# Kernel tuning notes

Measured on AMD Instinct MI355X. Metric: run time of the kernel, lower is better.

The kernel has to match this reference:

```python
import jax, jax.numpy as jnp
import numpy as np

D_MODEL = 512
N_HEADS = 8
HEAD_DIM = D_MODEL // N_HEADS
SCALE = float(np.sqrt(HEAD_DIM))


def setup_inputs() -> dict:
    key = jax.random.key(0)
    k1, k2, k3, k4, k5, k6 = jax.random.split(key, 6)
    B, T, S = 4, 2048, 4096
    query = jax.random.normal(k1, (B, T, D_MODEL), dtype=jnp.float32)
    keys = jax.random.normal(k2, (B, S, D_MODEL), dtype=jnp.float32)
    key_padding_mask = jnp.zeros((B, S), dtype=bool)  # all valid
    # Linear params (torch nn.Linear: y = x @ W.T + b)
    lim = 1.0 / np.sqrt(D_MODEL)
    q_w = jax.random.uniform(k3, (D_MODEL, D_MODEL), jnp.float32, -lim, lim)
    q_b = jax.random.uniform(k4, (D_MODEL,), jnp.float32, -lim, lim)
    k_w = jax.random.uniform(k5, (D_MODEL, D_MODEL), jnp.float32, -lim, lim)
    k_b = jax.random.uniform(k6, (D_MODEL,), jnp.float32, -lim, lim)
    return {"query": query, "keys": keys, "key_padding_mask": key_padding_mask,
            "q_w": q_w, "q_b": q_b, "k_w": k_w, "k_b": k_b}


def reference(query, keys, key_padding_mask, q_w, q_b, k_w, k_b):
    B, T, _ = query.shape
    S = keys.shape[1]
    q = (query @ q_w.T + q_b).reshape(B, T, N_HEADS, HEAD_DIM)
    k = (keys @ k_w.T + k_b).reshape(B, S, N_HEADS, HEAD_DIM)
    # mean over heads of scaled per-head QK^T == single contraction over (h,d)
    # divided by n_heads*scale; avoids materializing [B,H,T,S].
    logits = jnp.einsum('bthd,bshd->bts', q, k) / (N_HEADS * SCALE)
    logits = jnp.where(key_padding_mask[:, None, :], -jnp.inf, logits)
    return logits
```

## Files before the change

kernel.cpp:

```cpp
#include <hip/hip_runtime.h>
#include <hip/hip_bf16.h>

using bf16 = __hip_bfloat16;
typedef __attribute__((ext_vector_type(8))) short short8;
typedef __attribute__((ext_vector_type(4))) float floatx4;

#define NEG_INF (-__builtin_huge_valf())

__device__ __forceinline__ void gld_lds16(const void* g, void* l) {
  __builtin_amdgcn_global_load_lds(
      (const __attribute__((address_space(1))) unsigned int*)g,
      (__attribute__((address_space(3))) unsigned int*)l, 16, 0, 0);
}

__device__ __forceinline__ void cvt8(const float4& a, const float4& b, bf16* t) {
  t[0] = __float2bfloat16(a.x); t[1] = __float2bfloat16(a.y);
  t[2] = __float2bfloat16(a.z); t[3] = __float2bfloat16(a.w);
  t[4] = __float2bfloat16(b.x); t[5] = __float2bfloat16(b.y);
  t[6] = __float2bfloat16(b.z); t[7] = __float2bfloat16(b.w);
}

__global__ __launch_bounds__(256) void proj_fused(const float* __restrict__ X,
                                                  const float* __restrict__ Y,
                                                  const float* __restrict__ qw,
                                                  const float* __restrict__ kw,
                                                  const float* __restrict__ qb,
                                                  const float* __restrict__ kb,
                                                  bf16* __restrict__ qo,
                                                  bf16* __restrict__ ko) {
  __shared__ bf16 sA[128 * 32];
  __shared__ bf16 sB[128 * 32];
  const int mt = blockIdx.x;
  const bool isQ = mt < 64;
  const float* A    = isQ ? X  : Y;
  const float* W    = isQ ? qw : kw;
  const float* bias = isQ ? qb : kb;
  bf16* out         = isQ ? qo : ko;
  const int m0 = (isQ ? mt : mt - 64) * 128;
  const int n0 = blockIdx.y * 128;

  const int tid  = threadIdx.x;
  const int lane = tid & 63;
  const int w    = tid >> 6;
  const int wm   = (w >> 1) * 64;
  const int wn   = (w & 1) * 64;
  const int st_row = lane >> 2;
  const int st_col = (lane & 3) * 8;
  const int frag_m = lane & 15;
  const int frag_k = (lane >> 4) * 8;

  floatx4 acc[4][4];
  #pragma unroll
  for (int mi = 0; mi < 4; ++mi)
    #pragma unroll
    for (int ni = 0; ni < 4; ++ni)
      acc[mi][ni] = (floatx4){0.f, 0.f, 0.f, 0.f};

  for (int kt = 0; kt < 512; kt += 32) {
    #pragma unroll
    for (int j = 0; j < 2; ++j) {
      const int r = (w << 5) + (j << 4);
      const int row = r + st_row;
      const float* ga = A + (size_t)(m0 + row) * 512 + kt + st_col;
      const float* gb = W + (size_t)(n0 + row) * 512 + kt + st_col;
      float4 a0 = *(const float4*)ga;
      float4 a1 = *(const float4*)(ga + 4);
      float4 b0 = *(const float4*)gb;
      float4 b1 = *(const float4*)(gb + 4);
      bf16 ta[8], tb[8];
      cvt8(a0, a1, ta);
      cvt8(b0, b1, tb);
      *(short8*)(sA + row * 32 + st_col) = *(short8*)ta;
      *(short8*)(sB + row * 32 + st_col) = *(short8*)tb;
    }
    __syncthreads();

    short8 af[4], bfv[4];
    const bf16* pa = sA + (wm + frag_m) * 32 + frag_k;
    const bf16* pb = sB + (wn + frag_m) * 32 + frag_k;
    #pragma unroll
    for (int i = 0; i < 4; ++i) af[i]  = *(const short8*)(pa + i * 16 * 32);
    #pragma unroll
    for (int i = 0; i < 4; ++i) bfv[i] = *(const short8*)(pb + i * 16 * 32);
    #pragma unroll
    for (int mi = 0; mi < 4; ++mi)
      #pragma unroll
      for (int ni = 0; ni < 4; ++ni)
        acc[mi][ni] = __builtin_amdgcn_mfma_f32_16x16x32_bf16(af[mi], bfv[ni],
                                                              acc[mi][ni], 0, 0, 0);
    __syncthreads();
  }

  const int col = lane & 15;
  const int rbase = (lane >> 4) * 4;
  #pragma unroll
  for (int ni = 0; ni < 4; ++ni) {
    const int gn = n0 + wn + ni * 16 + col;
    const float b = bias[gn];
    #pragma unroll
    for (int mi = 0; mi < 4; ++mi) {
      const int gm = m0 + wm + mi * 16 + rbase;
      #pragma unroll
      for (int r = 0; r < 4; ++r)
        out[(size_t)(gm + r) * 512 + gn] = __float2bfloat16(acc[mi][ni][r] + b);
    }
  }
}

__global__ __launch_bounds__(256) void qk_gemm(const bf16* __restrict__ Q,
                                               const bf16* __restrict__ Kp,
                                               const unsigned char* __restrict__ mask,
                                               float* __restrict__ out) {
  __shared__ bf16 sA[128 * 32];
  __shared__ bf16 sB[128 * 32];
  const int b = blockIdx.z;
  const bf16* A  = Q  + (size_t)b * 2048 * 512;
  const bf16* Bm = Kp + (size_t)b * 4096 * 512;
  float* ob = out + (size_t)b * 2048 * 4096;
  const unsigned char* mb = mask + (size_t)b * 4096;
  const int m0 = blockIdx.x * 128;
  const int n0 = blockIdx.y * 128;

  const int tid  = threadIdx.x;
  const int lane = tid & 63;
  const int w    = tid >> 6;
  const int wm   = (w >> 1) * 64;
  const int wn   = (w & 1) * 64;
  const int st_row = lane >> 2;
  const int st_col = (lane & 3) * 8;
  const int frag_m = lane & 15;
  const int frag_k = (lane >> 4) * 8;

  floatx4 acc[4][4];
  #pragma unroll
  for (int mi = 0; mi < 4; ++mi)
    #pragma unroll
    for (int ni = 0; ni < 4; ++ni)
      acc[mi][ni] = (floatx4){0.f, 0.f, 0.f, 0.f};

  for (int kt = 0; kt < 512; kt += 32) {
    #pragma unroll
    for (int j = 0; j < 2; ++j) {
      const int r = (w << 5) + (j << 4);
      const bf16* ga = A  + (size_t)(m0 + r + st_row) * 512 + kt + st_col;
      const bf16* gb = Bm + (size_t)(n0 + r + st_row) * 512 + kt + st_col;
      gld_lds16(ga, sA + r * 32);
      gld_lds16(gb, sB + r * 32);
    }
    __syncthreads();

    short8 af[4], bfv[4];
    const bf16* pa = sA + (wm + frag_m) * 32 + frag_k;
    const bf16* pb = sB + (wn + frag_m) * 32 + frag_k;
    #pragma unroll
    for (int i = 0; i < 4; ++i) af[i]  = *(const short8*)(pa + i * 16 * 32);
    #pragma unroll
    for (int i = 0; i < 4; ++i) bfv[i] = *(const short8*)(pb + i * 16 * 32);
    #pragma unroll
    for (int mi = 0; mi < 4; ++mi)
      #pragma unroll
      for (int ni = 0; ni < 4; ++ni)
        acc[mi][ni] = __builtin_amdgcn_mfma_f32_16x16x32_bf16(af[mi], bfv[ni],
                                                              acc[mi][ni], 0, 0, 0);
    __syncthreads();
  }

  const int col = lane & 15;
  const int rbase = (lane >> 4) * 4;
  const float scale = 1.0f / 64.0f;
  #pragma unroll
  for (int ni = 0; ni < 4; ++ni) {
    const int gn = n0 + wn + ni * 16 + col;
    const bool msk = mb[gn] != 0;
    #pragma unroll
    for (int mi = 0; mi < 4; ++mi) {
      const int gm = m0 + wm + mi * 16 + rbase;
      #pragma unroll
      for (int r = 0; r < 4; ++r)
        ob[(size_t)(gm + r) * 4096 + gn] = msk ? NEG_INF : acc[mi][ni][r] * scale;
    }
  }
}

extern "C" void kernel_launch(void* const* d_in, const int* in_sizes, int n_in,
                              void* d_out, int out_size, void* d_ws, size_t ws_size,
                              hipStream_t stream) {
  const float* query = (const float*)d_in[0];
  const float* keys  = (const float*)d_in[1];
  const unsigned char* mask = (const unsigned char*)d_in[2];
  const float* q_w = (const float*)d_in[3];
  const float* q_b = (const float*)d_in[4];
  const float* k_w = (const float*)d_in[5];
  const float* k_b = (const float*)d_in[6];
  float* out = (float*)d_out;

  const int B = 4, T = 2048, S = 4096, D = 512;
  const int nq = B * T * D;
  const int nk = B * S * D;

  char* ws = (char*)d_ws;
  bf16* q_proj = (bf16*)(ws);
  bf16* k_proj = (bf16*)(ws + (size_t)nq * 2);

  proj_fused<<<dim3(192, D / 128), 256, 0, stream>>>(query, keys, q_w, k_w,
                                                     q_b, k_b, q_proj, k_proj);
  qk_gemm<<<dim3(T / 128, S / 128, B), 256, 0, stream>>>(q_proj, k_proj, mask, out);
}
```

Before: 239.7 us.

## Pre-convert weights to bf16 and double the K-step per barrier in both GEMMs

Adds a small kernel that converts the Q and K weight matrices to bf16 in workspace once per call. The projection GEMM can then load weights directly to LDS with global_load_lds instead of loading fp32 and converting each tile. Both GEMMs now stage two 32-wide K slices per iteration, which halves the number of barrier pairs at the cost of doubling the shared memory per block. This adds one extra kernel launch, and the larger LDS footprint may lower occupancy.

Result: no change. 241.8 us (+0.9%).

```diff
diff --git a/kernel.cpp b/kernel.cpp
--- a/kernel.cpp
+++ b/kernel.cpp
@@ -20,20 +20,33 @@
   t[6] = __float2bfloat16(b.z); t[7] = __float2bfloat16(b.w);
 }
 
+__global__ void cvt_w(const float* __restrict__ qw, const float* __restrict__ kw,
+                      bf16* __restrict__ qwo, bf16* __restrict__ kwo) {
+  const int i = blockIdx.x * blockDim.x + threadIdx.x;
+  const long e = (long)i << 3;
+  const float* src = (e < 262144) ? qw + e : kw + (e - 262144);
+  bf16*        dst = (e < 262144) ? qwo + e : kwo + (e - 262144);
+  float4 a = *(const float4*)src;
+  float4 b = *(const float4*)(src + 4);
+  bf16 t[8];
+  cvt8(a, b, t);
+  *(short8*)dst = *(short8*)t;
+}
+
 __global__ __launch_bounds__(256) void proj_fused(const float* __restrict__ X,
                                                   const float* __restrict__ Y,
-                                                  const float* __restrict__ qw,
-                                                  const float* __restrict__ kw,
+                                                  const bf16* __restrict__ qw,
+                                                  const bf16* __restrict__ kw,
                                                   const float* __restrict__ qb,
                                                   const float* __restrict__ kb,
                                                   bf16* __restrict__ qo,
                                                   bf16* __restrict__ ko) {
-  __shared__ bf16 sA[128 * 32];
-  __shared__ bf16 sB[128 * 32];
+  __shared__ bf16 sA[2][128 * 32];
+  __shared__ bf16 sB[2][128 * 32];
   const int mt = blockIdx.x;
   const bool isQ = mt < 64;
   const float* A    = isQ ? X  : Y;
-  const float* W    = isQ ? qw : kw;
+  const bf16*  W    = isQ ? qw : kw;
   const float* bias = isQ ? qb : kb;
   bf16* out         = isQ ? qo : ko;
   const int m0 = (isQ ? mt : mt - 64) * 128;
@@ -56,38 +69,45 @@
     for (int ni = 0; ni < 4; ++ni)
       acc[mi][ni] = (floatx4){0.f, 0.f, 0.f, 0.f};
 
-  for (int kt = 0; kt < 512; kt += 32) {
-    #pragma unroll
-    for (int j = 0; j < 2; ++j) {
-      const int r = (w << 5) + (j << 4);
-      const int row = r + st_row;
-      const float* ga = A + (size_t)(m0 + row) * 512 + kt + st_col;
-      const float* gb = W + (size_t)(n0 + row) * 512 + kt + st_col;
-      float4 a0 = *(const float4*)ga;
-      float4 a1 = *(const float4*)(ga + 4);
-      float4 b0 = *(const float4*)gb;
-      float4 b1 = *(const float4*)(gb + 4);
-      bf16 ta[8], tb[8];
-      cvt8(a0, a1, ta);
-      cvt8(b0, b1, tb);
-      *(short8*)(sA + row * 32 + st_col) = *(short8*)ta;
-      *(short8*)(sB + row * 32 + st_col) = *(short8*)tb;
-    }
-    __syncthreads();
-
-    short8 af[4], bfv[4];
-    const bf16* pa = sA + (wm + frag_m) * 32 + frag_k;
-    const bf16* pb = sB + (wn + frag_m) * 32 + frag_k;
-    #pragma unroll
-    for (int i = 0; i < 4; ++i) af[i]  = *(const short8*)(pa + i * 16 * 32);
-    #pragma unroll
-    for (int i = 0; i < 4; ++i) bfv[i] = *(const short8*)(pb + i * 16 * 32);
-    #pragma unroll
-    for (int mi = 0; mi < 4; ++mi)
-      #pragma unroll
-      for (int ni = 0; ni < 4; ++ni)
-        acc[mi][ni] = __builtin_amdgcn_mfma_f32_16x16x32_bf16(af[mi], bfv[ni],
-                                                              acc[mi][ni], 0, 0, 0);
+  for (int kt = 0; kt < 512; kt += 64) {
+    #pragma unroll
+    for (int h = 0; h < 2; ++h)
+      #pragma unroll
+      for (int j = 0; j < 2; ++j) {
+        const int r = (w << 5) + (j << 4);
+        const bf16* gb = W + (size_t)(n0 + r + st_row) * 512 + kt + h * 32 + st_col;
+        gld_lds16(gb, &sB[h][r * 32]);
+      }
+    #pragma unroll
+    for (int h = 0; h < 2; ++h)
+      #pragma unroll
+      for (int j = 0; j < 2; ++j) {
+        const int row = (w << 5) + (j << 4) + st_row;
+        const float* ga = A + (size_t)(m0 + row) * 512 + kt + h * 32 + st_col;
+        float4 a0 = *(const float4*)ga;
+        float4 a1 = *(const float4*)(ga + 4);
+        bf16 ta[8];
+        cvt8(a0, a1, ta);
+        *(short8*)(&sA[h][row * 32 + st_col]) = *(short8*)ta;
+      }
+    __syncthreads();
+
+    #pragma unroll
+    for (int h = 0; h < 2; ++h) {
+      short8 af[4], bfv[4];
+      const bf16* pa = &sA[h][(wm + frag_m) * 32 + frag_k];
+      const bf16* pb = &sB[h][(wn + frag_m) * 32 + frag_k];
+      #pragma unroll
+      for (int i = 0; i < 4; ++i) af[i]  = *(const short8*)(pa + i * 16 * 32);
+      #pragma unroll
+      for (int i = 0; i < 4; ++i) bfv[i] = *(const short8*)(pb + i * 16 * 32);
+      #pragma unroll
+      for (int mi = 0; mi < 4; ++mi)
+        #pragma unroll
+        for (int ni = 0; ni < 4; ++ni)
+          acc[mi][ni] = __builtin_amdgcn_mfma_f32_16x16x32_bf16(af[mi], bfv[ni],
+                                                                acc[mi][ni], 0, 0, 0);
+    }
     __syncthreads();
   }
 
@@ -111,8 +131,8 @@
                                                const bf16* __restrict__ Kp,
                                                const unsigned char* __restrict__ mask,
                                                float* __restrict__ out) {
-  __shared__ bf16 sA[128 * 32];
-  __shared__ bf16 sB[128 * 32];
+  __shared__ bf16 sA[2][128 * 32];
+  __shared__ bf16 sB[2][128 * 32];
   const int b = blockIdx.z;
   const bf16* A  = Q  + (size_t)b * 2048 * 512;
   const bf16* Bm = Kp + (size_t)b * 4096 * 512;
@@ -138,30 +158,35 @@
     for (int ni = 0; ni < 4; ++ni)
       acc[mi][ni] = (floatx4){0.f, 0.f, 0.f, 0.f};
 
-  for (int kt = 0; kt < 512; kt += 32) {
-    #pragma unroll
-    for (int j = 0; j < 2; ++j) {
-      const int r = (w << 5) + (j << 4);
-      const bf16* ga = A  + (size_t)(m0 + r + st_row) * 512 + kt + st_col;
-      const bf16* gb = Bm + (size_t)(n0 + r + st_row) * 512 + kt + st_col;
-      gld_lds16(ga, sA + r * 32);
-      gld_lds16(gb, sB + r * 32);
-    }
-    __syncthreads();
-
-    short8 af[4], bfv[4];
-    const bf16* pa = sA + (wm + frag_m) * 32 + frag_k;
-    const bf16* pb = sB + (wn + frag_m) * 32 + frag_k;
-    #pragma unroll
-    for (int i = 0; i < 4; ++i) af[i]  = *(const short8*)(pa + i * 16 * 32);
-    #pragma unroll
-    for (int i = 0; i < 4; ++i) bfv[i] = *(const short8*)(pb + i * 16 * 32);
-    #pragma unroll
-    for (int mi = 0; mi < 4; ++mi)
-      #pragma unroll
-      for (int ni = 0; ni < 4; ++ni)
-        acc[mi][ni] = __builtin_amdgcn_mfma_f32_16x16x32_bf16(af[mi], bfv[ni],
-                                                              acc[mi][ni], 0, 0, 0);
+  for (int kt = 0; kt < 512; kt += 64) {
+    #pragma unroll
+    for (int h = 0; h < 2; ++h)
+      #pragma unroll
+      for (int j = 0; j < 2; ++j) {
+        const int r = (w << 5) + (j << 4);
+        const bf16* ga = A  + (size_t)(m0 + r + st_row) * 512 + kt + h * 32 + st_col;
+        const bf16* gb = Bm + (size_t)(n0 + r + st_row) * 512 + kt + h * 32 + st_col;
+        gld_lds16(ga, &sA[h][r * 32]);
+        gld_lds16(gb, &sB[h][r * 32]);
+      }
+    __syncthreads();
+
+    #pragma unroll
+    for (int h = 0; h < 2; ++h) {
+      short8 af[4], bfv[4];
+      const bf16* pa = &sA[h][(wm + frag_m) * 32 + frag_k];
+      const bf16* pb = &sB[h][(wn + frag_m) * 32 + frag_k];
+      #pragma unroll
+      for (int i = 0; i < 4; ++i) af[i]  = *(const short8*)(pa + i * 16 * 32);
+      #pragma unroll
+      for (int i = 0; i < 4; ++i) bfv[i] = *(const short8*)(pb + i * 16 * 32);
+      #pragma unroll
+      for (int mi = 0; mi < 4; ++mi)
+        #pragma unroll
+        for (int ni = 0; ni < 4; ++ni)
+          acc[mi][ni] = __builtin_amdgcn_mfma_f32_16x16x32_bf16(af[mi], bfv[ni],
+                                                                acc[mi][ni], 0, 0, 0);
+    }
     __syncthreads();
   }
 
@@ -197,12 +222,16 @@
   const int B = 4, T = 2048, S = 4096, D = 512;
   const int nq = B * T * D;
   const int nk = B * S * D;
+  const int nw = D * D;
 
   char* ws = (char*)d_ws;
   bf16* q_proj = (bf16*)(ws);
   bf16* k_proj = (bf16*)(ws + (size_t)nq * 2);
-
-  proj_fused<<<dim3(192, D / 128), 256, 0, stream>>>(query, keys, q_w, k_w,
+  bf16* qw_bf  = (bf16*)(ws + (size_t)(nq + nk) * 2);
+  bf16* kw_bf  = (bf16*)(ws + (size_t)(nq + nk + nw) * 2);
+
+  cvt_w<<<256, 256, 0, stream>>>(q_w, k_w, qw_bf, kw_bf);
+  proj_fused<<<dim3(192, D / 128), 256, 0, stream>>>(query, keys, qw_bf, kw_bf,
                                                      q_b, k_b, q_proj, k_proj);
   qk_gemm<<<dim3(T / 128, S / 128, B), 256, 0, stream>>>(q_proj, k_proj, mask, out);
 }
```
